# Kernel tuning notes

Measured on AMD Instinct MI355X. Metric: run time of the kernel, lower is better.

Reference implementation:

```python
import jax, jax.numpy as jnp
import numpy as np

N = 200_000   # nodes per type
F_IN = 64     # input features per node type
H = 8         # hidden_channels (heads=1)
E = 3_000_000 # edges per edge type


def setup_inputs() -> dict:
    key = jax.random.key(0)
    ks = jax.random.split(key, 40)
    d = {}
    d['x_ind'] = jax.random.normal(ks[0], (N, F_IN), jnp.float32)
    d['x_org'] = jax.random.normal(ks[1], (N, F_IN), jnp.float32)
    d['x_ext'] = jax.random.normal(ks[2], (N, F_IN), jnp.float32)
    d['ei_ind_org'] = jax.random.randint(ks[3], (2, E), 0, N, jnp.int32)
    d['ei_org_ind'] = jax.random.randint(ks[4], (2, E), 0, N, jnp.int32)
    d['ei_ext_ind'] = jax.random.randint(ks[5], (2, E), 0, N, jnp.int32)
    d['ei_ext_org'] = jax.random.randint(ks[6], (2, E), 0, N, jnp.int32)
    s_in = 1.0 / np.sqrt(F_IN)
    # per-node-type projections (Linear(F_IN, H) with bias)
    for i, nt in enumerate(('ind', 'org', 'ext')):
        d[f'W_{nt}'] = jax.random.normal(ks[7 + i], (F_IN, H), jnp.float32) * s_in
        d[f'b_{nt}'] = jnp.zeros((H,), jnp.float32)
    # per-edge-type GAT attention vectors (heads=1, so shape [H])
    for i, et in enumerate(('ind_org', 'org_ind', 'ext_ind', 'ext_org')):
        d[f'att_src_{et}'] = jax.random.normal(ks[10 + 2 * i], (H,), jnp.float32) * (1.0 / np.sqrt(H))
        d[f'att_dst_{et}'] = jax.random.normal(ks[11 + 2 * i], (H,), jnp.float32) * (1.0 / np.sqrt(H))
    # semantic attention: k_lin(H->H) + query q
    d['k_W'] = jax.random.normal(ks[20], (H, H), jnp.float32) * (1.0 / np.sqrt(H))
    d['k_b'] = jnp.zeros((H,), jnp.float32)
    d['q'] = jax.random.normal(ks[21], (H,), jnp.float32)
    # prediction heads
    d['lin_ind_W'] = jax.random.normal(ks[22], (H, 1), jnp.float32) * (1.0 / np.sqrt(H))
    d['lin_ind_b'] = jnp.zeros((1,), jnp.float32)
    d['lin_org_W'] = jax.random.normal(ks[23], (H, 1), jnp.float32) * (1.0 / np.sqrt(H))
    d['lin_org_b'] = jnp.zeros((1,), jnp.float32)
    return d


def _gat_edge(h_src, h_dst, a_src, a_dst, ei):
    """Per-edge-type GAT message passing with segment softmax over dst."""
    row, col = ei[0], ei[1]
    alpha_s = h_src @ a_src  # [N]
    alpha_d = h_dst @ a_dst  # [N]
    alpha = jax.nn.leaky_relu(alpha_s[row] + alpha_d[col], 0.2)  # [E]
    m = jax.lax.stop_gradient(jax.ops.segment_max(alpha, col, num_segments=N))
    m = jnp.where(jnp.isfinite(m), m, 0.0)
    ex = jnp.exp(alpha - m[col])
    den = jax.ops.segment_sum(ex, col, num_segments=N) + 1e-16
    w = ex / den[col]  # [E]
    out = jax.ops.segment_sum(h_src[row] * w[:, None], col, num_segments=N)  # [N,H]
    return jax.nn.relu(out)


def _group(outs, q, k_W, k_b):
    """Semantic-level attention over metapath embeddings."""
    o = jnp.stack(outs)  # [M, N, H]
    score = (jnp.tanh(o @ k_W + k_b) @ q).mean(axis=1)  # [M]
    attn = jax.nn.softmax(score)
    return jnp.einsum('m,mnf->nf', attn, o)


def reference(x_ind, x_org, x_ext,
              ei_ind_org, ei_org_ind, ei_ext_ind, ei_ext_org,
              W_ind, b_ind, W_org, b_org, W_ext, b_ext,
              att_src_ind_org, att_dst_ind_org,
              att_src_org_ind, att_dst_org_ind,
              att_src_ext_ind, att_dst_ext_ind,
              att_src_ext_org, att_dst_ext_org,
              k_W, k_b, q,
              lin_ind_W, lin_ind_b, lin_org_W, lin_org_b):
    h_ind = x_ind @ W_ind + b_ind  # [N,H]
    h_org = x_org @ W_org + b_org
    h_ext = x_ext @ W_ext + b_ext
    # metapaths into 'ind'
    outs_ind = [
        _gat_edge(h_org, h_ind, att_src_org_ind, att_dst_org_ind, ei_org_ind),
        _gat_edge(h_ext, h_ind, att_src_ext_ind, att_dst_ext_ind, ei_ext_ind),
    ]
    # metapaths into 'org'
    outs_org = [
        _gat_edge(h_ind, h_org, att_src_ind_org, att_dst_ind_org, ei_ind_org),
        _gat_edge(h_ext, h_org, att_src_ext_org, att_dst_ext_org, ei_ext_org),
    ]
    z_ind = _group(outs_ind, q, k_W, k_b)  # [N,H]
    z_org = _group(outs_org, q, k_W, k_b)
    pred_ind = jax.nn.sigmoid(z_ind @ lin_ind_W + lin_ind_b)[:, 0]
    pred_org = jax.nn.sigmoid(z_org @ lin_org_W + lin_org_b)[:, 0]
    return (pred_ind, pred_org)
```

## Files before the change

### kernel.cpp

```cpp
#include <hip/hip_runtime.h>
#include <hip/hip_fp16.h>

#define HH 8
#define FIN 64
#define CHUNK 8192
#define NPB 1024
#define NPB_SHIFT 10
#define MAXNB 256
#define SUBCH 4096

__device__ __forceinline__ float b2f(unsigned short u) {
  union { unsigned int i; float f; } x;
  x.i = ((unsigned int)u) << 16;
  return x.f;
}

__device__ __forceinline__ float lrelu(float x) { return x > 0.f ? x : 0.2f * x; }

__device__ __forceinline__ float ld(const void* p, int i, int isf) {
  return isf ? ((const float*)p)[i] : b2f(((const unsigned short*)p)[i]);
}

struct MP {
  const int* ei;
  const float* as;
  const float* ad;
  const __half* hs;
  float* den;
  float* out;
  uint2* sorted;
  int* gcur;
  int E;
  int nchunks;
  int rcap;
};
struct MP4 { MP m[4]; };

__global__ void detect_kernel(const unsigned short* __restrict__ x, int* __restrict__ flag) {
  __shared__ int s[256];
  int t = threadIdx.x;
  int cnt = 0;
  for (int i = t; i < 2048; i += 256) {
    int e = (x[i] >> 7) & 0xFF;
    if (e >= 0x90) cnt++;
  }
  s[t] = cnt;
  __syncthreads();
  for (int k = 128; k > 0; k >>= 1) {
    if (t < k) s[t] += s[t + k];
    __syncthreads();
  }
  if (t == 0) flag[0] = (s[0] >= 8) ? 1 : 0;
}

__global__ void fill_u32(unsigned int* __restrict__ p, long long n, unsigned int v) {
  long long i = (long long)blockIdx.x * blockDim.x + threadIdx.x;
  if (i < n) p[i] = v;
}

__global__ void init_cursors(int* __restrict__ g, int nslots, int rcap) {
  int i = blockIdx.x * blockDim.x + threadIdx.x;
  if (i < nslots * 256) g[i] = (i & 255) * rcap;
}

__global__ void proj_kernel(const void* __restrict__ x,
                            const void* __restrict__ W,
                            const void* __restrict__ b,
                            __half* __restrict__ h16, int N,
                            const void* __restrict__ a0v, float* __restrict__ s0,
                            const void* __restrict__ a1v, float* __restrict__ s1,
                            const void* __restrict__ a2v, float* __restrict__ s2,
                            const int* __restrict__ flag) {
  __shared__ float Wl[FIN][HH];
  __shared__ float bl[HH];
  __shared__ float al[3][HH];
  int isf = flag[0];
  int t = threadIdx.x;
  for (int i = t; i < FIN * HH; i += blockDim.x) Wl[i >> 3][i & 7] = ld(W, i, isf);
  if (t < HH) {
    bl[t] = ld(b, t, isf);
    al[0][t] = a0v ? ld(a0v, t, isf) : 0.f;
    al[1][t] = a1v ? ld(a1v, t, isf) : 0.f;
    al[2][t] = a2v ? ld(a2v, t, isf) : 0.f;
  }
  __syncthreads();
  int n = blockIdx.x * blockDim.x + t;
  if (n >= N) return;
  float acc[HH];
#pragma unroll
  for (int j = 0; j < HH; ++j) acc[j] = bl[j];
  if (isf) {
    const float4* xr = (const float4*)((const float*)x + (size_t)n * FIN);
#pragma unroll
    for (int v = 0; v < FIN / 4; ++v) {
      float4 p = xr[v];
      float f4[4] = {p.x, p.y, p.z, p.w};
#pragma unroll
      for (int k = 0; k < 4; ++k) {
        int f = v * 4 + k;
#pragma unroll
        for (int j = 0; j < HH; ++j) acc[j] += f4[k] * Wl[f][j];
      }
    }
  } else {
    const uint4* xr = (const uint4*)((const unsigned short*)x + (size_t)n * FIN);
#pragma unroll
    for (int v = 0; v < FIN / 8; ++v) {
      uint4 p = xr[v];
      unsigned int w[4] = {p.x, p.y, p.z, p.w};
#pragma unroll
      for (int k = 0; k < 4; ++k) {
        float f0 = __uint_as_float(w[k] << 16);
        float f1 = __uint_as_float(w[k] & 0xFFFF0000u);
        int f = v * 8 + k * 2;
#pragma unroll
        for (int j = 0; j < HH; ++j) acc[j] += f0 * Wl[f][j];
#pragma unroll
        for (int j = 0; j < HH; ++j) acc[j] += f1 * Wl[f + 1][j];
      }
    }
  }
  union { __half h[8]; uint4 u; } pk;
#pragma unroll
  for (int j = 0; j < HH; ++j) pk.h[j] = __float2half(acc[j]);
  *(uint4*)(h16 + (size_t)n * HH) = pk.u;
  float d0 = 0.f, d1 = 0.f, d2 = 0.f;
#pragma unroll
  for (int j = 0; j < HH; ++j) {
    d0 += acc[j] * al[0][j];
    d1 += acc[j] * al[1][j];
    d2 += acc[j] * al[2][j];
  }
  if (s0) s0[n] = d0;
  if (s1) s1[n] = d1;
  if (s2) s2[n] = d2;
}

__global__ void __launch_bounds__(512)
partA(MP4 a4, int mp_base, int NB) {
  const MP a = a4.m[mp_base + blockIdx.y];
  int k = blockIdx.x;
  if (k >= a.nchunks) return;
  __shared__ uint2 buf[CHUNK];
  __shared__ int cnt[MAXNB];
  __shared__ int cur[MAXNB];
  __shared__ int off[MAXNB];
  __shared__ int posArr[MAXNB];
  __shared__ int part[512];
  int t = threadIdx.x;
  int E = a.E;
  int base = k * CHUNK;
  int len = E - base; if (len > CHUNK) len = CHUNK;
  if (t < MAXNB) cnt[t] = 0;
  __syncthreads();
#pragma unroll
  for (int i = 0; i < 16; ++i) {
    int idx = i * 512 + t;
    if (idx < len) {
      int c = a.ei[E + base + idx];
      atomicAdd(&cnt[c >> NPB_SHIFT], 1);
    }
  }
  __syncthreads();
  int myc = (t < NB) ? cnt[t] : 0;
  if (t < NB && myc > 0) posArr[t] = atomicAdd(&a.gcur[t], myc);
  part[t] = myc;
  __syncthreads();
  for (int d = 1; d < 512; d <<= 1) {
    int v = (t >= d) ? part[t - d] : 0;
    __syncthreads();
    part[t] += v;
    __syncthreads();
  }
  if (t < NB) { off[t] = part[t] - myc; cur[t] = part[t] - myc; }
  __syncthreads();
  for (int hbat = 0; hbat < 2; ++hbat) {
    int rr[8], cc[8];
    float asv[8], adv[8];
#pragma unroll
    for (int j = 0; j < 8; ++j) {
      int idx = (hbat * 8 + j) * 512 + t;
      rr[j] = -1;
      if (idx < len) { rr[j] = a.ei[base + idx]; cc[j] = a.ei[E + base + idx]; }
    }
#pragma unroll
    for (int j = 0; j < 8; ++j) {
      if (rr[j] >= 0) { asv[j] = a.as[rr[j]]; adv[j] = a.ad[cc[j]]; }
    }
#pragma unroll
    for (int j = 0; j < 8; ++j) {
      if (rr[j] >= 0) {
        float ex = __expf(lrelu(asv[j] + adv[j]));
        int b = cc[j] >> NPB_SHIFT;
        int p = atomicAdd(&cur[b], 1);
        uint2 v;
        v.x = ((unsigned)(cc[j] & (NPB - 1)) << 22) | (unsigned)rr[j];
        v.y = __float_as_uint(ex);
        buf[p] = v;
      }
    }
  }
  __syncthreads();
  int wv = t >> 6, ln = t & 63;
  for (int s = wv; s < NB; s += 8) {
    int cn = cnt[s];
    if (cn == 0) continue;
    int c0 = off[s];
    int gb = posArr[s];
    int lim = (s + 1) * a.rcap;
    int mx = lim - gb; if (mx < 0) mx = 0;
    if (cn > mx) cn = mx;
    for (int j = ln; j < cn; j += 64) a.sorted[(size_t)gb + j] = buf[c0 + j];
  }
}

__global__ void __launch_bounds__(512)
partB(MP4 a4, int mp_base, int NB, int N, int fused) {
  int mp, b;
  if (fused) {
    int blk = blockIdx.x;
    int xcd = blk & 7;
    mp = xcd >> 1;
    b = ((blk >> 3) << 1) + (xcd & 1);
    if (b >= NB) return;
  } else {
    mp = mp_base;
    b = blockIdx.x;
  }
  const MP a = a4.m[mp];
  __shared__ uint2 key2[SUBCH];
  __shared__ int cnt2[NPB];
  __shared__ int o2[NPB];
  __shared__ int cur2[NPB];
  __shared__ int part[512];
  int t = threadIdx.x;
  int s0 = b * a.rcap;
  int cnt = a.gcur[b] - s0;
  if (cnt < 0) cnt = 0;
  if (cnt > a.rcap) cnt = a.rcap;
  const uint2* run = a.sorted + (size_t)s0;

  float acc0[HH], acc1[HH];
#pragma unroll
  for (int f = 0; f < HH; ++f) { acc0[f] = 0.f; acc1[f] = 0.f; }
  float dn0 = 0.f, dn1 = 0.f;
  const __half* hs = a.hs;

  for (int c0 = 0; c0 < cnt; c0 += SUBCH) {
    int m = cnt - c0; if (m > SUBCH) m = SUBCH;
    cnt2[t] = 0; cnt2[t + 512] = 0;
    __syncthreads();
    uint2 kk[8];
    int vld[8];
#pragma unroll
    for (int u = 0; u < 8; ++u) {
      int idx = u * 512 + t;
      vld[u] = idx < m;
      if (vld[u]) kk[u] = run[c0 + idx];
    }
#pragma unroll
    for (int u = 0; u < 8; ++u) {
      if (vld[u]) atomicAdd(&cnt2[kk[u].x >> 22], 1);
    }
    __syncthreads();
    int a0 = cnt2[2 * t], a1 = cnt2[2 * t + 1];
    int sm = a0 + a1;
    part[t] = sm;
    __syncthreads();
    for (int d = 1; d < 512; d <<= 1) {
      int v = (t >= d) ? part[t - d] : 0;
      __syncthreads();
      part[t] += v;
      __syncthreads();
    }
    int ex = part[t] - sm;
    o2[2 * t] = ex;       cur2[2 * t] = ex;
    o2[2 * t + 1] = ex + a0; cur2[2 * t + 1] = ex + a0;
    __syncthreads();
#pragma unroll
    for (int u = 0; u < 8; ++u) {
      if (vld[u]) {
        int p = atomicAdd(&cur2[kk[u].x >> 22], 1);
        key2[p] = kk[u];
      }
    }
    __syncthreads();
    {
      int n = t;
      int j = o2[n], e = cur2[n];
      for (; j < e; ++j) {
        uint2 v = key2[j];
        float w = __uint_as_float(v.y);
        union { uint4 u; __half h[8]; } H;
        H.u = *(const uint4*)(hs + (size_t)(v.x & 0x3FFFFFu) * HH);
        dn0 += w;
#pragma unroll
        for (int f = 0; f < HH; ++f) acc0[f] += w * __half2float(H.h[f]);
      }
    }
    {
      int n = t + 512;
      int j = o2[n], e = cur2[n];
      for (; j < e; ++j) {
        uint2 v = key2[j];
        float w = __uint_as_float(v.y);
        union { uint4 u; __half h[8]; } H;
        H.u = *(const uint4*)(hs + (size_t)(v.x & 0x3FFFFFu) * HH);
        dn1 += w;
#pragma unroll
        for (int f = 0; f < HH; ++f) acc1[f] += w * __half2float(H.h[f]);
      }
    }
    __syncthreads();
  }
  int basen = b << NPB_SHIFT;
  {
    int node = basen + t;
    if (node < N) {
      float4* po = (float4*)(a.out + (size_t)node * HH);
      po[0] = make_float4(acc0[0], acc0[1], acc0[2], acc0[3]);
      po[1] = make_float4(acc0[4], acc0[5], acc0[6], acc0[7]);
      a.den[node] = dn0;
    }
  }
  {
    int node = basen + t + 512;
    if (node < N) {
      float4* po = (float4*)(a.out + (size_t)node * HH);
      po[0] = make_float4(acc1[0], acc1[1], acc1[2], acc1[3]);
      po[1] = make_float4(acc1[4], acc1[5], acc1[6], acc1[7]);
      a.den[node] = dn1;
    }
  }
}

__global__ void score_kernel(const float* __restrict__ o0, const float* __restrict__ d0,
                             const float* __restrict__ o1, const float* __restrict__ d1,
                             int N,
                             const void* __restrict__ kW,
                             const void* __restrict__ kb,
                             const void* __restrict__ qv,
                             float* __restrict__ score,
                             const int* __restrict__ flag) {
  __shared__ float kWl[HH][HH];
  __shared__ float kbl[HH], ql[HH];
  __shared__ float red0[256], red1[256];
  int isf = flag[0];
  int t = threadIdx.x;
  if (t < HH * HH) kWl[t >> 3][t & 7] = ld(kW, t, isf);
  if (t < HH) { kbl[t] = ld(kb, t, isf); ql[t] = ld(qv, t, isf); }
  __syncthreads();
  int n = blockIdx.x * blockDim.x + t;
  float s0 = 0.f, s1 = 0.f;
  if (n < N) {
    const float* p0 = o0 + (size_t)n * HH;
    const float* p1 = o1 + (size_t)n * HH;
    float i0 = 1.f / (d0[n] + 1e-16f);
    float i1 = 1.f / (d1[n] + 1e-16f);
    float v0[HH], v1[HH];
#pragma unroll
    for (int j = 0; j < HH; ++j) { v0[j] = fmaxf(p0[j] * i0, 0.f); v1[j] = fmaxf(p1[j] * i1, 0.f); }
#pragma unroll
    for (int j = 0; j < HH; ++j) {
      float t0 = kbl[j], t1 = kbl[j];
#pragma unroll
      for (int i = 0; i < HH; ++i) { t0 += v0[i] * kWl[i][j]; t1 += v1[i] * kWl[i][j]; }
      s0 += tanhf(t0) * ql[j];
      s1 += tanhf(t1) * ql[j];
    }
  }
  red0[t] = s0; red1[t] = s1;
  __syncthreads();
  for (int s = 128; s > 0; s >>= 1) {
    if (t < s) { red0[t] += red0[t + s]; red1[t] += red1[t + s]; }
    __syncthreads();
  }
  if (t == 0) { atomicAdd(&score[0], red0[0]); atomicAdd(&score[1], red1[0]); }
}

__global__ void pred_kernel(const float* __restrict__ o0, const float* __restrict__ d0,
                            const float* __restrict__ o1, const float* __restrict__ d1,
                            int N,
                            const float* __restrict__ score,
                            const void* __restrict__ linW,
                            const void* __restrict__ linb,
                            float* __restrict__ outp,
                            const int* __restrict__ flag) {
  int isf = flag[0];
  int n = blockIdx.x * blockDim.x + threadIdx.x;
  if (n >= N) return;
  float s0 = score[0] / (float)N, s1 = score[1] / (float)N;
  float mx = fmaxf(s0, s1);
  float e0 = __expf(s0 - mx), e1 = __expf(s1 - mx);
  float inv = 1.f / (e0 + e1);
  float a0 = e0 * inv, a1 = e1 * inv;
  const float* p0 = o0 + (size_t)n * HH;
  const float* p1 = o1 + (size_t)n * HH;
  float i0 = 1.f / (d0[n] + 1e-16f);
  float i1 = 1.f / (d1[n] + 1e-16f);
  float acc = ld(linb, 0, isf);
#pragma unroll
  for (int j = 0; j < HH; ++j) {
    float z = a0 * fmaxf(p0[j] * i0, 0.f) + a1 * fmaxf(p1[j] * i1, 0.f);
    acc += z * ld(linW, j, isf);
  }
  outp[n] = 1.f / (1.f + __expf(-acc));
}

extern "C" void kernel_launch(void* const* d_in, const int* in_sizes, int n_in,
                              void* d_out, int out_size, void* d_ws, size_t ws_size,
                              hipStream_t stream) {
  const int N = in_sizes[0] / FIN;

  const void* x_ind = d_in[0];
  const void* x_org = d_in[1];
  const void* x_ext = d_in[2];
  const int* ei_io = (const int*)d_in[3];  int E_io = in_sizes[3] / 2;
  const int* ei_oi = (const int*)d_in[4];  int E_oi = in_sizes[4] / 2;
  const int* ei_ei = (const int*)d_in[5];  int E_ei = in_sizes[5] / 2;
  const int* ei_eo = (const int*)d_in[6];  int E_eo = in_sizes[6] / 2;
  const void* W_ind = d_in[7];
  const void* b_ind = d_in[8];
  const void* W_org = d_in[9];
  const void* b_org = d_in[10];
  const void* W_ext = d_in[11];
  const void* b_ext = d_in[12];
  const void* att_src_io = d_in[13];
  const void* att_dst_io = d_in[14];
  const void* att_src_oi = d_in[15];
  const void* att_dst_oi = d_in[16];
  const void* att_src_ei = d_in[17];
  const void* att_dst_ei = d_in[18];
  const void* att_src_eo = d_in[19];
  const void* att_dst_eo = d_in[20];
  const void* k_W = d_in[21];
  const void* k_b = d_in[22];
  const void* qv  = d_in[23];
  const void* lin_ind_W = d_in[24];
  const void* lin_ind_b = d_in[25];
  const void* lin_org_W = d_in[26];
  const void* lin_org_b = d_in[27];

  float* out_f = (float*)d_out;

  int E_max = E_io;
  if (E_oi > E_max) E_max = E_oi;
  if (E_ei > E_max) E_max = E_ei;
  if (E_eo > E_max) E_max = E_eo;

  const int NB = (N + NPB - 1) >> NPB_SHIFT;
  const int nchunks_max = (E_max + CHUNK - 1) / CHUNK;
  const int rcap = (int)(((long long)E_max / NB) * 115 / 100) + 128;

  float* ws = (float*)d_ws;
  size_t off = 0;
  __half* h16_ind = (__half*)(ws + off); off += (size_t)N * HH / 2;
  __half* h16_org = (__half*)(ws + off); off += (size_t)N * HH / 2;
  __half* h16_ext = (__half*)(ws + off); off += (size_t)N * HH / 2;
  float* as_io = ws + off; off += N;
  float* ad_oi = ws + off; off += N;
  float* ad_ei = ws + off; off += N;
  float* as_oi = ws + off; off += N;
  float* ad_io = ws + off; off += N;
  float* ad_eo = ws + off; off += N;
  float* as_ei = ws + off; off += N;
  float* as_eo = ws + off; off += N;
  float* den_all = ws + off; off += (size_t)4 * N;
  float* out_all = ws + off; off += (size_t)4 * N * HH;
  float* score_all = ws + off; off += 4;
  int* flag = (int*)(ws + off); off += 1;
  off = (off + 1) & ~(size_t)1;
  int* gcur0 = (int*)(ws + off); off += 4 * 256;

  size_t sort_f = (size_t)2 * NB * rcap;
  bool big = (off + 4 * sort_f) * sizeof(float) <= ws_size;
  int slots = big ? 4 : 1;
  uint2* sorted0 = (uint2*)(ws + off); off += (size_t)slots * sort_f;

  const int BS = 256;
  const int nb_node = (N + BS - 1) / BS;

  detect_kernel<<<1, BS, 0, stream>>>((const unsigned short*)x_ind, flag);
  fill_u32<<<1, BS, 0, stream>>>((unsigned int*)score_all, 4, 0u);

  proj_kernel<<<nb_node, BS, 0, stream>>>(x_ind, W_ind, b_ind, h16_ind, N,
                                          att_src_io, as_io, att_dst_oi, ad_oi, att_dst_ei, ad_ei, flag);
  proj_kernel<<<nb_node, BS, 0, stream>>>(x_org, W_org, b_org, h16_org, N,
                                          att_src_oi, as_oi, att_dst_io, ad_io, att_dst_eo, ad_eo, flag);
  proj_kernel<<<nb_node, BS, 0, stream>>>(x_ext, W_ext, b_ext, h16_ext, N,
                                          att_src_ei, as_ei, att_src_eo, as_eo,
                                          (const void*)nullptr, (float*)nullptr, flag);

  const int* eis[4]       = {ei_oi, ei_ei, ei_io, ei_eo};
  int        Es[4]        = {E_oi, E_ei, E_io, E_eo};
  const float* ass[4]     = {as_oi, as_ei, as_io, as_eo};
  const float* ads[4]     = {ad_oi, ad_ei, ad_io, ad_eo};
  const __half* hsrcs[4]  = {h16_org, h16_ext, h16_ind, h16_ext};

  MP4 a4;
  for (int mp = 0; mp < 4; ++mp) {
    MP& a = a4.m[mp];
    a.ei = eis[mp];
    a.as = ass[mp];
    a.ad = ads[mp];
    a.hs = hsrcs[mp];
    a.den = den_all + (size_t)mp * N;
    a.out = out_all + (size_t)mp * N * HH;
    a.sorted = (uint2*)((float*)sorted0 + (size_t)(big ? mp : 0) * sort_f);
    a.gcur = gcur0 + (big ? mp : 0) * 256;
    a.E = Es[mp];
    a.nchunks = (Es[mp] + CHUNK - 1) / CHUNK;
    a.rcap = rcap;
  }

  if (big) {
    init_cursors<<<4, 256, 0, stream>>>(gcur0, 4, rcap);
    partA<<<dim3(nchunks_max, 4), 512, 0, stream>>>(a4, 0, NB);
    int nblkB = 8 * ((NB + 1) >> 1);
    partB<<<dim3(nblkB, 1), 512, 0, stream>>>(a4, 0, NB, N, 1);
  } else {
    for (int mp = 0; mp < 4; ++mp) {
      init_cursors<<<1, 256, 0, stream>>>(a4.m[mp].gcur, 1, rcap);
      partA<<<dim3(a4.m[mp].nchunks, 1), 512, 0, stream>>>(a4, mp, NB);
      partB<<<dim3(NB, 1), 512, 0, stream>>>(a4, mp, NB, N, 0);
    }
  }

  float* o_ind0 = out_all + (size_t)0 * N * HH;
  float* o_ind1 = out_all + (size_t)1 * N * HH;
  float* o_org0 = out_all + (size_t)2 * N * HH;
  float* o_org1 = out_all + (size_t)3 * N * HH;
  float* d_ind0 = den_all + (size_t)0 * N;
  float* d_ind1 = den_all + (size_t)1 * N;
  float* d_org0 = den_all + (size_t)2 * N;
  float* d_org1 = den_all + (size_t)3 * N;

  score_kernel<<<nb_node, BS, 0, stream>>>(o_ind0, d_ind0, o_ind1, d_ind1, N,
                                           k_W, k_b, qv, score_all, flag);
  score_kernel<<<nb_node, BS, 0, stream>>>(o_org0, d_org0, o_org1, d_org1, N,
                                           k_W, k_b, qv, score_all + 2, flag);

  pred_kernel<<<nb_node, BS, 0, stream>>>(o_ind0, d_ind0, o_ind1, d_ind1, N, score_all,
                                          lin_ind_W, lin_ind_b, out_f, flag);
  pred_kernel<<<nb_node, BS, 0, stream>>>(o_org0, d_org0, o_org1, d_org1, N, score_all + 2,
                                          lin_org_W, lin_org_b, out_f + N, flag);
}
```

Measured before the change: 649.9 us.

## Replace shared-memory scans with wave shuffles, pad LDS bins, prefetch next subchunk

In the edge-bucketing pass, blocks shrink to 256 threads over 4096-edge chunks. Each thread loads its edge indices once and keeps them in registers instead of reading them twice. The multi-barrier Hillis-Steele prefix scans in both passes become a single-wave __shfl_up scan. Shared-memory counter arrays are padded every 32 entries to reduce bank conflicts, and the second pass prefetches the next subchunk's keys while aggregating the current one. Together these aim to cut barrier count, redundant global loads and LDS conflicts, at the cost of more registers and twice as many first-pass blocks.

```diff
diff --git a/kernel.cpp b/kernel.cpp
--- a/kernel.cpp
+++ b/kernel.cpp
@@ -3,11 +3,12 @@
 
 #define HH 8
 #define FIN 64
-#define CHUNK 8192
+#define CHUNK 4096
 #define NPB 1024
 #define NPB_SHIFT 10
 #define MAXNB 256
 #define SUBCH 4096
+#define PADI(i) ((i) + ((i) >> 5))
 
 __device__ __forceinline__ float b2f(unsigned short u) {
   union { unsigned int i; float f; } x;
@@ -136,65 +137,72 @@
   if (s2) s2[n] = d2;
 }
 
-__global__ void __launch_bounds__(512)
+__global__ void __launch_bounds__(256)
 partA(MP4 a4, int mp_base, int NB) {
   const MP a = a4.m[mp_base + blockIdx.y];
   int k = blockIdx.x;
   if (k >= a.nchunks) return;
   __shared__ uint2 buf[CHUNK];
-  __shared__ int cnt[MAXNB];
-  __shared__ int cur[MAXNB];
-  __shared__ int off[MAXNB];
-  __shared__ int posArr[MAXNB];
-  __shared__ int part[512];
+  __shared__ int cnt[264];
+  __shared__ int cur[264];
+  __shared__ int off[264];
+  __shared__ int posA[264];
   int t = threadIdx.x;
   int E = a.E;
   int base = k * CHUNK;
   int len = E - base; if (len > CHUNK) len = CHUNK;
-  if (t < MAXNB) cnt[t] = 0;
-  __syncthreads();
-#pragma unroll
-  for (int i = 0; i < 16; ++i) {
-    int idx = i * 512 + t;
-    if (idx < len) {
-      int c = a.ei[E + base + idx];
-      atomicAdd(&cnt[c >> NPB_SHIFT], 1);
-    }
-  }
-  __syncthreads();
-  int myc = (t < NB) ? cnt[t] : 0;
-  if (t < NB && myc > 0) posArr[t] = atomicAdd(&a.gcur[t], myc);
-  part[t] = myc;
-  __syncthreads();
-  for (int d = 1; d < 512; d <<= 1) {
-    int v = (t >= d) ? part[t - d] : 0;
-    __syncthreads();
-    part[t] += v;
-    __syncthreads();
-  }
-  if (t < NB) { off[t] = part[t] - myc; cur[t] = part[t] - myc; }
-  __syncthreads();
-  for (int hbat = 0; hbat < 2; ++hbat) {
-    int rr[8], cc[8];
+  for (int i = t; i < 264; i += 256) cnt[i] = 0;
+  __syncthreads();
+  int rr[16], cc[16];
+#pragma unroll
+  for (int j = 0; j < 16; ++j) {
+    int idx = j * 256 + t;
+    rr[j] = -1;
+    if (idx < len) { rr[j] = a.ei[base + idx]; cc[j] = a.ei[E + base + idx]; }
+  }
+#pragma unroll
+  for (int j = 0; j < 16; ++j)
+    if (rr[j] >= 0) atomicAdd(&cnt[PADI(cc[j] >> NPB_SHIFT)], 1);
+  __syncthreads();
+  if (t < 64) {
+    int b0 = t * 4;
+    int c0 = cnt[PADI(b0)], c1 = cnt[PADI(b0 + 1)];
+    int c2 = cnt[PADI(b0 + 2)], c3 = cnt[PADI(b0 + 3)];
+    int s = c0 + c1 + c2 + c3;
+    int inc = s;
+#pragma unroll
+    for (int d = 1; d < 64; d <<= 1) {
+      int v = __shfl_up(inc, d, 64);
+      if (t >= d) inc += v;
+    }
+    int run = inc - s;
+    int o0 = run, o1 = o0 + c0, o2v = o1 + c1, o3 = o2v + c2;
+    off[PADI(b0)] = o0;     cur[PADI(b0)] = o0;
+    off[PADI(b0 + 1)] = o1; cur[PADI(b0 + 1)] = o1;
+    off[PADI(b0 + 2)] = o2v; cur[PADI(b0 + 2)] = o2v;
+    off[PADI(b0 + 3)] = o3; cur[PADI(b0 + 3)] = o3;
+    posA[PADI(b0)]     = c0 ? atomicAdd(&a.gcur[b0], c0) : 0;
+    posA[PADI(b0 + 1)] = c1 ? atomicAdd(&a.gcur[b0 + 1], c1) : 0;
+    posA[PADI(b0 + 2)] = c2 ? atomicAdd(&a.gcur[b0 + 2], c2) : 0;
+    posA[PADI(b0 + 3)] = c3 ? atomicAdd(&a.gcur[b0 + 3], c3) : 0;
+  }
+  __syncthreads();
+  for (int hb = 0; hb < 2; ++hb) {
     float asv[8], adv[8];
 #pragma unroll
     for (int j = 0; j < 8; ++j) {
-      int idx = (hbat * 8 + j) * 512 + t;
-      rr[j] = -1;
-      if (idx < len) { rr[j] = a.ei[base + idx]; cc[j] = a.ei[E + base + idx]; }
+      int i = hb * 8 + j;
+      if (rr[i] >= 0) { asv[j] = a.as[rr[i]]; adv[j] = a.ad[cc[i]]; }
     }
 #pragma unroll
     for (int j = 0; j < 8; ++j) {
-      if (rr[j] >= 0) { asv[j] = a.as[rr[j]]; adv[j] = a.ad[cc[j]]; }
-    }
-#pragma unroll
-    for (int j = 0; j < 8; ++j) {
-      if (rr[j] >= 0) {
+      int i = hb * 8 + j;
+      if (rr[i] >= 0) {
         float ex = __expf(lrelu(asv[j] + adv[j]));
-        int b = cc[j] >> NPB_SHIFT;
-        int p = atomicAdd(&cur[b], 1);
+        int bb = cc[i] >> NPB_SHIFT;
+        int p = atomicAdd(&cur[PADI(bb)], 1);
         uint2 v;
-        v.x = ((unsigned)(cc[j] & (NPB - 1)) << 22) | (unsigned)rr[j];
+        v.x = ((unsigned)(cc[i] & (NPB - 1)) << 22) | (unsigned)rr[i];
         v.y = __float_as_uint(ex);
         buf[p] = v;
       }
@@ -202,11 +210,11 @@
   }
   __syncthreads();
   int wv = t >> 6, ln = t & 63;
-  for (int s = wv; s < NB; s += 8) {
-    int cn = cnt[s];
+  for (int s = wv; s < NB; s += 4) {
+    int cn = cnt[PADI(s)];
     if (cn == 0) continue;
-    int c0 = off[s];
-    int gb = posArr[s];
+    int c0 = off[PADI(s)];
+    int gb = posA[PADI(s)];
     int lim = (s + 1) * a.rcap;
     int mx = lim - gb; if (mx < 0) mx = 0;
     if (cn > mx) cn = mx;
@@ -229,10 +237,9 @@
   }
   const MP a = a4.m[mp];
   __shared__ uint2 key2[SUBCH];
-  __shared__ int cnt2[NPB];
-  __shared__ int o2[NPB];
-  __shared__ int cur2[NPB];
-  __shared__ int part[512];
+  __shared__ int cnt2[1056];
+  __shared__ int o2[1056];
+  __shared__ int cur2[1056];
   int t = threadIdx.x;
   int s0 = b * a.rcap;
   int cnt = a.gcur[b] - s0;
@@ -246,48 +253,67 @@
   float dn0 = 0.f, dn1 = 0.f;
   const __half* hs = a.hs;
 
-  for (int c0 = 0; c0 < cnt; c0 += SUBCH) {
-    int m = cnt - c0; if (m > SUBCH) m = SUBCH;
-    cnt2[t] = 0; cnt2[t + 512] = 0;
-    __syncthreads();
-    uint2 kk[8];
-    int vld[8];
+  uint2 kk[8];
+  int vld[8];
+  {
+    int m0 = cnt < SUBCH ? cnt : SUBCH;
 #pragma unroll
     for (int u = 0; u < 8; ++u) {
       int idx = u * 512 + t;
-      vld[u] = idx < m;
-      if (vld[u]) kk[u] = run[c0 + idx];
-    }
-#pragma unroll
-    for (int u = 0; u < 8; ++u) {
-      if (vld[u]) atomicAdd(&cnt2[kk[u].x >> 22], 1);
-    }
-    __syncthreads();
-    int a0 = cnt2[2 * t], a1 = cnt2[2 * t + 1];
-    int sm = a0 + a1;
-    part[t] = sm;
-    __syncthreads();
-    for (int d = 1; d < 512; d <<= 1) {
-      int v = (t >= d) ? part[t - d] : 0;
-      __syncthreads();
-      part[t] += v;
-      __syncthreads();
-    }
-    int ex = part[t] - sm;
-    o2[2 * t] = ex;       cur2[2 * t] = ex;
-    o2[2 * t + 1] = ex + a0; cur2[2 * t + 1] = ex + a0;
+      vld[u] = idx < m0;
+      if (vld[u]) kk[u] = run[idx];
+    }
+  }
+
+  for (int c0 = 0; c0 < cnt; c0 += SUBCH) {
+    for (int i = t; i < 1056; i += 512) cnt2[i] = 0;
+    __syncthreads();
+#pragma unroll
+    for (int u = 0; u < 8; ++u)
+      if (vld[u]) atomicAdd(&cnt2[PADI(kk[u].x >> 22)], 1);
+    __syncthreads();
+    if (t < 64) {
+      int c[16];
+      int s = 0;
+#pragma unroll
+      for (int j = 0; j < 16; ++j) { c[j] = cnt2[PADI(t * 16 + j)]; s += c[j]; }
+      int inc = s;
+#pragma unroll
+      for (int d = 1; d < 64; d <<= 1) {
+        int v = __shfl_up(inc, d, 64);
+        if (t >= d) inc += v;
+      }
+      int run2 = inc - s;
+#pragma unroll
+      for (int j = 0; j < 16; ++j) {
+        o2[PADI(t * 16 + j)] = run2;
+        cur2[PADI(t * 16 + j)] = run2;
+        run2 += c[j];
+      }
+    }
     __syncthreads();
 #pragma unroll
     for (int u = 0; u < 8; ++u) {
       if (vld[u]) {
-        int p = atomicAdd(&cur2[kk[u].x >> 22], 1);
+        int p = atomicAdd(&cur2[PADI(kk[u].x >> 22)], 1);
         key2[p] = kk[u];
       }
     }
     __syncthreads();
+    int cn0 = c0 + SUBCH;
+    uint2 nk[8];
+    int nv[8];
     {
-      int n = t;
-      int j = o2[n], e = cur2[n];
+      int mn = cnt - cn0; if (mn > SUBCH) mn = SUBCH;
+#pragma unroll
+      for (int u = 0; u < 8; ++u) {
+        int idx = u * 512 + t;
+        nv[u] = (cn0 < cnt) && (idx < mn);
+        if (nv[u]) nk[u] = run[(size_t)cn0 + idx];
+      }
+    }
+    {
+      int j = o2[PADI(t)], e = cur2[PADI(t)];
       for (; j < e; ++j) {
         uint2 v = key2[j];
         float w = __uint_as_float(v.y);
@@ -299,8 +325,7 @@
       }
     }
     {
-      int n = t + 512;
-      int j = o2[n], e = cur2[n];
+      int j = o2[PADI(t + 512)], e = cur2[PADI(t + 512)];
       for (; j < e; ++j) {
         uint2 v = key2[j];
         float w = __uint_as_float(v.y);
@@ -312,6 +337,8 @@
       }
     }
     __syncthreads();
+#pragma unroll
+    for (int u = 0; u < 8; ++u) { vld[u] = nv[u]; kk[u] = nk[u]; }
   }
   int basen = b << NPB_SHIFT;
   {
@@ -515,13 +542,13 @@
 
   if (big) {
     init_cursors<<<4, 256, 0, stream>>>(gcur0, 4, rcap);
-    partA<<<dim3(nchunks_max, 4), 512, 0, stream>>>(a4, 0, NB);
+    partA<<<dim3(nchunks_max, 4), 256, 0, stream>>>(a4, 0, NB);
     int nblkB = 8 * ((NB + 1) >> 1);
     partB<<<dim3(nblkB, 1), 512, 0, stream>>>(a4, 0, NB, N, 1);
   } else {
     for (int mp = 0; mp < 4; ++mp) {
       init_cursors<<<1, 256, 0, stream>>>(a4.m[mp].gcur, 1, rcap);
-      partA<<<dim3(a4.m[mp].nchunks, 1), 512, 0, stream>>>(a4, mp, NB);
+      partA<<<dim3(a4.m[mp].nchunks, 1), 256, 0, stream>>>(a4, mp, NB);
       partB<<<dim3(NB, 1), 512, 0, stream>>>(a4, mp, NB, N, 0);
     }
   }
```

New measurement: 692.4 us. 1.07x slower.
